# Kernel tuning notes

Hardware: AMD Instinct MI355X
Metric: run time of the kernel (lower is better)

Reference implementation:

```python
import jax, jax.numpy as jnp
import numpy as np

DT = 0.01  # integration timestep of the Euler-discretized plant


def setup_inputs() -> dict:
    key = jax.random.key(0)
    ks = jax.random.split(key, 8)
    B, T, n, m, c = 2048, 128, 16, 8, 4
    state0 = jax.random.normal(ks[0], (B, n), dtype=jnp.float32)
    controls = jax.random.normal(ks[1], (B, T, c), dtype=jnp.float32)
    obs = jax.random.normal(ks[2], (B, T, m), dtype=jnp.float32)
    A = jax.random.normal(ks[3], (n, n), dtype=jnp.float32) * 0.3
    Bc = jax.random.normal(ks[4], (n, c), dtype=jnp.float32)
    H = jax.random.normal(ks[5], (m, n), dtype=jnp.float32) * 0.5
    Mq = jax.random.normal(ks[6], (n, n), dtype=jnp.float32)
    Q = (Mq @ Mq.T) * (0.01 / n) + 0.01 * jnp.eye(n, dtype=jnp.float32)  # SPD process noise
    Mr = jax.random.normal(ks[7], (m, m), dtype=jnp.float32)
    R = (Mr @ Mr.T) * (0.1 / m) + 0.1 * jnp.eye(m, dtype=jnp.float32)    # SPD obs noise
    P0 = jnp.broadcast_to(jnp.eye(n, dtype=jnp.float32), (B, n, n))       # initial covariance
    return {"state0": state0, "P0": P0, "controls": controls, "obs": obs,
            "A": A, "Bc": Bc, "H": H, "Q": Q, "R": R}


def reference(state0, P0, controls, obs, A, Bc, H, Q, R):
    # Batched Kalman filter (predict + update) over T steps, then RTS smoothing.
    B, n = state0.shape
    T = controls.shape[1]
    I = jnp.eye(n, dtype=state0.dtype)
    F = I + DT * A  # constant Jacobian of the linear Euler plant

    def plant(s, u):  # s: [B,n], u: [B,c]
        return s + DT * (s @ A.T + u @ Bc.T)

    def filt_step(carry, xs):
        s_f, P_f = carry          # filtered state/cov from previous step
        u, y = xs                 # [B,c], [B,m]
        # --- prediction: state_ = plant(s), P_ = F P F^T + Q ---
        s_p = plant(s_f, u)
        P_p = jnp.einsum('ij,bjk,lk->bil', F, P_f, F) + Q
        # --- filtering: K = P H^T (H P H^T + R)^{-1} ---
        PHt = jnp.einsum('bij,kj->bik', P_p, H)       # [B,n,m]
        S = jnp.einsum('ki,bim->bkm', H, PHt) + R      # [B,m,m]
        K = PHt @ jnp.linalg.inv(S)                    # [B,n,m]
        innov = y - s_p @ H.T                          # obs - obs_pred
        s_new = s_p + jnp.einsum('bnm,bm->bn', K, innov)
        P_new = P_p - jnp.einsum('bnm,mj,bjk->bnk', K, H, P_p)
        return (s_new, P_new), (s_p, P_p, s_new, P_new)

    xs = (jnp.swapaxes(controls, 0, 1), jnp.swapaxes(obs, 0, 1))  # [T,B,...]
    _, (s_p_seq, P_p_seq, s_f_seq, P_f_seq) = jax.lax.scan(filt_step, (state0, P0), xs)

    # --- RTS smoothing: A = P_f F^T P_p^{-1}; backward recursion ---
    def smooth_step(carry, xs):
        s_s_next, P_s_next = carry
        s_f, P_f, s_p_next, P_p_next = xs
        Pinv = jnp.linalg.inv(P_p_next)
        G = jnp.einsum('bij,kj,bkl->bil', P_f, F, Pinv)   # smoothing gain [B,n,n]
        s_s = s_f + jnp.einsum('bnm,bm->bn', G, s_s_next - s_p_next)
        P_s = P_f + G @ (P_s_next - P_p_next) @ jnp.swapaxes(G, -1, -2)
        return (s_s, P_s), s_s

    xs_s = (s_f_seq[:-1], P_f_seq[:-1], s_p_seq[1:], P_p_seq[1:])
    init = (s_f_seq[-1], P_f_seq[-1])
    _, s_s_seq = jax.lax.scan(smooth_step, init, xs_s, reverse=True)
    s_s_all = jnp.concatenate([s_s_seq, s_f_seq[-1:]], axis=0)  # [T,B,n]
    return jnp.swapaxes(s_s_all, 0, 1)  # smoothed states [B,T,n]
```

## Files before the change

### kernel.cpp

```cpp
#include <hip/hip_runtime.h>

#define NB 2048
#define TS 128
#define NS 16
#define MS 8
#define CS 4
#define DTC 0.01f

#define K_OFF 0
#define K_SZ (TS*NS*MS)
#define G_OFF (K_OFF + K_SZ)
#define G_SZ ((TS-1)*NS*NS)
#define PP_OFF (G_OFF + G_SZ)
#define PP_SZ (TS*NS*NS)
#define PF_OFF (PP_OFF + PP_SZ)
#define PF_SZ (TS*NS*NS)
#define A_OFF (PF_OFF + PF_SZ)
#define A_SZ (TS*NS*NS)
#define M_OFF (A_OFF + A_SZ)
#define M_SZ (TS*NS*CS)

#define GSHFL(v, k) __shfl((v), ((tid & 48) | (k)), 64)

__global__ __launch_bounds__(256) void cov_kernel(
    const float* __restrict__ Ag, const float* __restrict__ Hg,
    const float* __restrict__ Qg, const float* __restrict__ Rg,
    const float* __restrict__ P0g, const float* __restrict__ Bcg,
    float* __restrict__ Kw, float* __restrict__ Ppw, float* __restrict__ Pfw,
    float* __restrict__ Aw, float* __restrict__ Mw)
{
    __shared__ float Fs[NS][NS], Qs[NS][NS];
    __shared__ float Hs[MS][NS], HFs[MS][NS], QHt[NS][MS];
    __shared__ float Rs[MS][MS], HBcs[MS][CS], Bcs[NS][CS];
    __shared__ float Pf[NS][NS], Pp[NS][NS], TP[NS][NS];
    __shared__ float PHt[NS][MS], HP[MS][NS], Ks[NS][MS];
    __shared__ float Sg[MS][MS];

    const int tid = threadIdx.x;
    const int i = tid >> 4, j = tid & 15;

    float Fri[NS];
#pragma unroll
    for (int k = 0; k < NS; ++k) Fri[k] = ((i == k) ? 1.f : 0.f) + DTC * Ag[i*NS + k];

    Fs[i][j] = ((i == j) ? 1.f : 0.f) + DTC * Ag[tid];
    Qs[i][j] = Qg[tid];
    if (tid < MS*NS) Hs[tid >> 4][tid & 15] = Hg[tid];
    if (tid < MS*MS) Rs[tid >> 3][tid & 7] = Rg[tid];
    if (tid < NS*CS) Bcs[tid >> 2][tid & 3] = Bcg[tid];
    Pf[i][j] = P0g[tid];
    __syncthreads();

    if (tid < MS*NS) {
        const int a = tid >> 4, k = tid & 15;
        float acc = 0.f;
#pragma unroll
        for (int m = 0; m < NS; ++m) acc += Hs[a][m] * Fs[m][k];
        HFs[a][k] = acc;
    } else {
        const int e = tid - 128, ii = e >> 3, b = e & 7;
        float acc = 0.f;
#pragma unroll
        for (int k = 0; k < NS; ++k) acc += Qs[ii][k] * Hs[b][k];
        QHt[ii][b] = acc;
    }
    if (tid < MS*CS) {
        const int r = tid >> 2, c = tid & 3;
        float acc = 0.f;
#pragma unroll
        for (int k = 0; k < NS; ++k) acc += Hs[r][k] * Bcs[k][c];
        HBcs[r][c] = acc;
    }
    __syncthreads();

    for (int t = 0; t < TS; ++t) {
        {
            float a0 = 0.f, a1 = 0.f;
#pragma unroll
            for (int k = 0; k < NS; k += 2) { a0 += Fri[k]*Pf[k][j]; a1 += Fri[k+1]*Pf[k+1][j]; }
            TP[i][j] = a0 + a1;
        }
        __syncthreads();

        if (tid < NS*MS) {
            const int ii = tid >> 3, l = tid & 7;
            float b0 = QHt[ii][l], b1 = 0.f;
#pragma unroll
            for (int k = 0; k < NS; k += 2) { b0 += TP[ii][k]*HFs[l][k]; b1 += TP[ii][k+1]*HFs[l][k+1]; }
            PHt[ii][l] = b0 + b1;
        } else {
            const int e = tid - 128;
#pragma unroll
            for (int rep = 0; rep < 2; ++rep) {
                const int en = e + rep*128;
                const int ie = en >> 4, je = en & 15;
                float c0 = Qs[ie][je], c1 = 0.f;
#pragma unroll
                for (int k = 0; k < NS; k += 2) { c0 += TP[ie][k]*Fs[je][k]; c1 += TP[ie][k+1]*Fs[je][k+1]; }
                const float ppv = c0 + c1;
                Pp[ie][je] = ppv;
                Ppw[t*(NS*NS) + en] = ppv;
            }
        }
        __syncthreads();

        if (tid < 64) {
            const int r = tid >> 3, c = tid & 7;
            float v = Rs[r][c];
#pragma unroll
            for (int k = 0; k < NS; ++k) v += Hs[r][k] * PHt[k][c];
            Sg[r][c] = v;
        } else if (tid >= 128) {
            const int e = tid - 128, m = e >> 4, jj = e & 15;
            float v = 0.f;
#pragma unroll
            for (int k = 0; k < NS; ++k) v += Hs[m][k] * Pp[k][jj];
            HP[m][jj] = v;
        }
        __syncthreads();

        if (tid < 128) {
            const int ii = tid >> 3, m = tid & 7;
            float Sr[MS][MS];
#pragma unroll
            for (int a = 0; a < MS; ++a) {
                const float4 x0 = *(const float4*)&Sg[a][0];
                const float4 x1 = *(const float4*)&Sg[a][4];
                Sr[a][0]=x0.x; Sr[a][1]=x0.y; Sr[a][2]=x0.z; Sr[a][3]=x0.w;
                Sr[a][4]=x1.x; Sr[a][5]=x1.y; Sr[a][6]=x1.z; Sr[a][7]=x1.w;
            }
            float rds[MS];
#pragma unroll
            for (int p = 0; p < MS; ++p) {
                const float rd = 1.f / Sr[p][p]; rds[p] = rd;
#pragma unroll
                for (int r = p+1; r < MS; ++r) {
                    const float f = Sr[r][p] * rd; Sr[r][p] = f;
#pragma unroll
                    for (int c = p+1; c < MS; ++c) Sr[r][c] -= f * Sr[p][c];
                }
            }
            float yv[MS];
#pragma unroll
            for (int r = 0; r < MS; ++r) {
                float v = (r == m) ? 1.f : 0.f;
#pragma unroll
                for (int c = 0; c < r; ++c) v -= Sr[r][c] * yv[c];
                yv[r] = v;
            }
            float xv[MS];
#pragma unroll
            for (int r = MS-1; r >= 0; --r) {
                float v = yv[r];
#pragma unroll
                for (int c = r+1; c < MS; ++c) v -= Sr[r][c] * xv[c];
                xv[r] = v * rds[r];
            }
            const float4 p0 = *(const float4*)&PHt[ii][0];
            const float4 p1 = *(const float4*)&PHt[ii][4];
            float kv = p0.x*xv[0] + p0.y*xv[1] + p0.z*xv[2] + p0.w*xv[3]
                     + p1.x*xv[4] + p1.y*xv[5] + p1.z*xv[6] + p1.w*xv[7];
            Ks[ii][m] = kv;
            Kw[t*(NS*MS) + tid] = kv;
        }
        __syncthreads();

        {
            float kr[MS];
            *(float4*)&kr[0] = *(const float4*)&Ks[i][0];
            *(float4*)&kr[4] = *(const float4*)&Ks[i][4];
            float pf = Pp[i][j], av = Fs[i][j];
#pragma unroll
            for (int m = 0; m < MS; ++m) { pf -= kr[m] * HP[m][j]; av -= kr[m] * HFs[m][j]; }
            Pf[i][j] = pf;
            Pfw[t*(NS*NS) + tid] = pf;
            Aw[t*(NS*NS) + tid] = av;
            if (tid < NS*CS) {
                const int ri = tid >> 2, c = tid & 3;
                float mv = Bcs[ri][c];
#pragma unroll
                for (int m = 0; m < MS; ++m) mv -= Ks[ri][m] * HBcs[m][c];
                Mw[t*(NS*CS) + tid] = DTC * mv;
            }
        }
        __syncthreads();
    }
}

__global__ __launch_bounds__(256) void g_kernel(
    const float* __restrict__ Ag,
    const float* __restrict__ Ppw, const float* __restrict__ Pfw,
    float* __restrict__ Gw)
{
    const int t   = blockIdx.x;
    const int tid = threadIdx.x;
    const int r = tid >> 4, cl = tid & 15;

    __shared__ float aug0[NS][NS], aug1[NS][NS], Pfs[NS][NS], Ws[NS][NS];

    float Frc[NS];
#pragma unroll
    for (int k = 0; k < NS; ++k) Frc[k] = ((cl == k) ? 1.f : 0.f) + DTC * Ag[cl*NS + k];

    aug0[r][cl] = Ppw[(t+1)*(NS*NS) + tid];
    aug1[r][cl] = (r == cl) ? 1.f : 0.f;
    Pfs[r][cl]  = Pfw[t*(NS*NS) + tid];
    __syncthreads();

    for (int p = 0; p < NS; ++p) {
        const float a0 = aug0[r][cl], a1 = aug1[r][cl];
        const float d  = aug0[p][p];
        const float pa = aug0[p][cl], pb = aug1[p][cl];
        const float f  = aug0[r][p];
        __syncthreads();
        const float rd = 1.f / d;
        if (r == p) { aug0[r][cl] = pa * rd;       aug1[r][cl] = pb * rd; }
        else        { const float frd = f * rd;
                      aug0[r][cl] = a0 - frd * pa; aug1[r][cl] = a1 - frd * pb; }
        __syncthreads();
    }

    float w0 = 0.f, w1 = 0.f;
#pragma unroll
    for (int k = 0; k < NS; k += 2) { w0 += Pfs[r][k]*Frc[k]; w1 += Pfs[r][k+1]*Frc[k+1]; }
    Ws[r][cl] = w0 + w1;
    __syncthreads();

    float g0 = 0.f, g1 = 0.f;
#pragma unroll
    for (int k = 0; k < NS; k += 2) { g0 += Ws[r][k]*aug1[k][cl]; g1 += Ws[r][k+1]*aug1[k+1][cl]; }
    Gw[t*(NS*NS) + tid] = g0 + g1;
}

__global__ __launch_bounds__(256) void prep_kernel(
    const float* __restrict__ ctrl, const float* __restrict__ obsg,
    const float* __restrict__ Kw, const float* __restrict__ Mw,
    float* __restrict__ outp)
{
    const int g = blockIdx.x * 256 + threadIdx.x;
    const int b = g >> 11;
    const int rem = g & 2047;
    const int t = rem >> 4, i = rem & 15;

    const float4 u  = *(const float4*)(ctrl + (size_t)b*TS*CS + t*CS);
    const float4 y0 = *(const float4*)(obsg + (size_t)b*TS*MS + t*MS);
    const float4 y1 = *(const float4*)(obsg + (size_t)b*TS*MS + t*MS + 4);
    const float4 mr = *(const float4*)(Mw + t*(NS*CS) + i*CS);
    const float4 k0 = *(const float4*)(Kw + t*(NS*MS) + i*MS);
    const float4 k1 = *(const float4*)(Kw + t*(NS*MS) + i*MS + 4);

    float v = mr.x*u.x + mr.y*u.y + mr.z*u.z + mr.w*u.w;
    v += k0.x*y0.x + k0.y*y0.y + k0.z*y0.z + k0.w*y0.w;
    v += k1.x*y1.x + k1.y*y1.y + k1.z*y1.z + k1.w*y1.w;
    outp[g] = v;
}

__global__ __launch_bounds__(256) void fwd_kernel(
    const float* __restrict__ s0g, const float* __restrict__ Aw,
    float* __restrict__ outp)
{
    const int tid  = threadIdx.x;
    const int lane = tid & 15;
    const int b    = blockIdx.x * 16 + (tid >> 4);

    float s = s0g[b*NS + lane];
    float* ob = outp + (size_t)b * TS * NS;

    float4 a0 = *(const float4*)(Aw + lane*NS);
    float4 a1 = *(const float4*)(Aw + lane*NS + 4);
    float4 a2 = *(const float4*)(Aw + lane*NS + 8);
    float4 a3 = *(const float4*)(Aw + lane*NS + 12);

    for (int t = 0; t < TS; ++t) {
        const float bt = ob[t*NS + lane];
        float4 n0, n1, n2, n3;
        if (t + 1 < TS) {
            const float* ap = Aw + (t+1)*(NS*NS) + lane*NS;
            n0 = *(const float4*)(ap);     n1 = *(const float4*)(ap + 4);
            n2 = *(const float4*)(ap + 8); n3 = *(const float4*)(ap + 12);
        }
        float p0 = bt, p1 = 0.f, p2 = 0.f, p3 = 0.f;
        p0 += a0.x*GSHFL(s,0)  + a0.y*GSHFL(s,1);
        p1 += a0.z*GSHFL(s,2)  + a0.w*GSHFL(s,3);
        p2 += a1.x*GSHFL(s,4)  + a1.y*GSHFL(s,5);
        p3 += a1.z*GSHFL(s,6)  + a1.w*GSHFL(s,7);
        p0 += a2.x*GSHFL(s,8)  + a2.y*GSHFL(s,9);
        p1 += a2.z*GSHFL(s,10) + a2.w*GSHFL(s,11);
        p2 += a3.x*GSHFL(s,12) + a3.y*GSHFL(s,13);
        p3 += a3.z*GSHFL(s,14) + a3.w*GSHFL(s,15);
        const float sn = (p0 + p1) + (p2 + p3);
        ob[t*NS + lane] = sn;
        s = sn;
        if (t + 1 < TS) { a0 = n0; a1 = n1; a2 = n2; a3 = n3; }
    }
}

__global__ __launch_bounds__(256) void bwd_kernel(
    const float* __restrict__ Gw, const float* __restrict__ ctrl,
    const float* __restrict__ Ag, const float* __restrict__ Bcg,
    float* __restrict__ outp)
{
    const int tid  = threadIdx.x;
    const int lane = tid & 15;
    const int b    = blockIdx.x * 16 + (tid >> 4);

    float Fi[NS], Bci[CS];
#pragma unroll
    for (int k = 0; k < NS; ++k) Fi[k] = ((lane == k) ? 1.f : 0.f) + DTC * Ag[lane*NS + k];
#pragma unroll
    for (int k = 0; k < CS; ++k) Bci[k] = DTC * Bcg[lane*CS + k];

    const float* up = ctrl + (size_t)b * TS * CS;
    float* ob = outp + (size_t)b * TS * NS;

    float ss = ob[(TS-1)*NS + lane];

    for (int t = TS-2; t >= 0; --t) {
        const float sf = ob[t*NS + lane];

        const float4 u = *(const float4*)(up + (t+1)*CS);
        float p0 = Bci[0]*u.x + Bci[1]*u.y, p1 = Bci[2]*u.z + Bci[3]*u.w, p2 = 0.f, p3 = 0.f;
#pragma unroll
        for (int k = 0; k < NS; k += 4) {
            p0 += Fi[k  ] * GSHFL(sf, k);
            p1 += Fi[k+1] * GSHFL(sf, k+1);
            p2 += Fi[k+2] * GSHFL(sf, k+2);
            p3 += Fi[k+3] * GSHFL(sf, k+3);
        }
        const float diff = ss - ((p0 + p1) + (p2 + p3));

        const float4 g0 = *(const float4*)(Gw + t*(NS*NS) + lane*NS);
        const float4 g1 = *(const float4*)(Gw + t*(NS*NS) + lane*NS + 4);
        const float4 g2 = *(const float4*)(Gw + t*(NS*NS) + lane*NS + 8);
        const float4 g3 = *(const float4*)(Gw + t*(NS*NS) + lane*NS + 12);

        float a0 = g0.x*GSHFL(diff,0)  + g0.y*GSHFL(diff,1);
        a0      += g0.z*GSHFL(diff,2)  + g0.w*GSHFL(diff,3);
        float a1 = g1.x*GSHFL(diff,4)  + g1.y*GSHFL(diff,5);
        a1      += g1.z*GSHFL(diff,6)  + g1.w*GSHFL(diff,7);
        float a2 = g2.x*GSHFL(diff,8)  + g2.y*GSHFL(diff,9);
        a2      += g2.z*GSHFL(diff,10) + g2.w*GSHFL(diff,11);
        float a3 = g3.x*GSHFL(diff,12) + g3.y*GSHFL(diff,13);
        a3      += g3.z*GSHFL(diff,14) + g3.w*GSHFL(diff,15);

        const float sn = sf + ((a0 + a1) + (a2 + a3));
        ob[t*NS + lane] = sn;
        ss = sn;
    }
}

extern "C" void kernel_launch(void* const* d_in, const int* in_sizes, int n_in,
                              void* d_out, int out_size, void* d_ws, size_t ws_size,
                              hipStream_t stream)
{
    (void)out_size; (void)ws_size;

    const float *s0 = nullptr, *P0 = nullptr, *ctrl = nullptr, *obs = nullptr;
    const float *A = nullptr, *Bc = nullptr, *H = nullptr, *Q = nullptr, *R = nullptr;
    for (int idx = 0; idx < n_in; ++idx) {
        const float* p = (const float*)d_in[idx];
        switch (in_sizes[idx]) {
            case NB*NS:        s0   = p; break;
            case NB*NS*NS:     P0   = p; break;
            case NB*TS*CS:     ctrl = p; break;
            case NB*TS*MS:     obs  = p; break;
            case MS*NS:        H    = p; break;
            case NS*NS:        if (!A)  A  = p; else Q = p; break;
            case MS*MS:        if (!Bc) Bc = p; else R = p; break;
            default: break;
        }
    }

    float* ws  = (float*)d_ws;
    float* Kw  = ws + K_OFF;
    float* Gw  = ws + G_OFF;
    float* Ppw = ws + PP_OFF;
    float* Pfw = ws + PF_OFF;
    float* Aw  = ws + A_OFF;
    float* Mw  = ws + M_OFF;
    float* out = (float*)d_out;

    hipLaunchKernelGGL(cov_kernel,  dim3(1),            dim3(256), 0, stream,
                       A, H, Q, R, P0, Bc, Kw, Ppw, Pfw, Aw, Mw);
    hipLaunchKernelGGL(g_kernel,    dim3(TS-1),         dim3(256), 0, stream, A, Ppw, Pfw, Gw);
    hipLaunchKernelGGL(prep_kernel, dim3(NB*TS*NS/256), dim3(256), 0, stream, ctrl, obs, Kw, Mw, out);
    hipLaunchKernelGGL(fwd_kernel,  dim3(NB/16),        dim3(256), 0, stream, s0, Aw, out);
    hipLaunchKernelGGL(bwd_kernel,  dim3(NB/16),        dim3(256), 0, stream, Gw, ctrl, A, Bc, out);
}
```

Baseline: 360.9 us.

## Shorten covariance step dependency chain and prefetch per-step loads in scans

The covariance kernel now computes the innovation covariance S directly from the filtered covariance, as HF·Pf·(HF)^T + (H Q H^T + R). The constant term is precomputed once as Rbar. This removes one barrier-separated phase per timestep, and the HP product moves into the idle threads of the solve phase. The forward and backward state kernels also prefetch the next timestep's value from global memory one iteration ahead, hiding load latency on the serial recurrence. The reassociated S is algebraically equivalent but may differ slightly in rounding.

```diff
diff --git a/kernel.cpp b/kernel.cpp
--- a/kernel.cpp
+++ b/kernel.cpp
@@ -31,8 +31,8 @@
 {
     __shared__ float Fs[NS][NS], Qs[NS][NS];
     __shared__ float Hs[MS][NS], HFs[MS][NS], QHt[NS][MS];
-    __shared__ float Rs[MS][MS], HBcs[MS][CS], Bcs[NS][CS];
-    __shared__ float Pf[NS][NS], Pp[NS][NS], TP[NS][NS];
+    __shared__ float Rs[MS][MS], Rbar[MS][MS], HBcs[MS][CS], Bcs[NS][CS];
+    __shared__ float Pf[NS][NS], Pp[NS][NS], TP[NS][NS], Ws[MS][NS];
     __shared__ float PHt[NS][MS], HP[MS][NS], Ks[NS][MS];
     __shared__ float Sg[MS][MS];
 
@@ -73,49 +73,51 @@
     }
     __syncthreads();
 
+    if (tid < MS*MS) {
+        const int r = tid >> 3, c = tid & 7;
+        float acc = Rs[r][c];
+#pragma unroll
+        for (int k = 0; k < NS; ++k) acc += Hs[r][k] * QHt[k][c];
+        Rbar[r][c] = acc;
+    }
+    __syncthreads();
+
     for (int t = 0; t < TS; ++t) {
         {
             float a0 = 0.f, a1 = 0.f;
 #pragma unroll
             for (int k = 0; k < NS; k += 2) { a0 += Fri[k]*Pf[k][j]; a1 += Fri[k+1]*Pf[k+1][j]; }
             TP[i][j] = a0 + a1;
-        }
-        __syncthreads();
-
-        if (tid < NS*MS) {
-            const int ii = tid >> 3, l = tid & 7;
-            float b0 = QHt[ii][l], b1 = 0.f;
-#pragma unroll
-            for (int k = 0; k < NS; k += 2) { b0 += TP[ii][k]*HFs[l][k]; b1 += TP[ii][k+1]*HFs[l][k+1]; }
-            PHt[ii][l] = b0 + b1;
-        } else {
-            const int e = tid - 128;
-#pragma unroll
-            for (int rep = 0; rep < 2; ++rep) {
-                const int en = e + rep*128;
-                const int ie = en >> 4, je = en & 15;
-                float c0 = Qs[ie][je], c1 = 0.f;
-#pragma unroll
-                for (int k = 0; k < NS; k += 2) { c0 += TP[ie][k]*Fs[je][k]; c1 += TP[ie][k+1]*Fs[je][k+1]; }
-                const float ppv = c0 + c1;
-                Pp[ie][je] = ppv;
-                Ppw[t*(NS*NS) + en] = ppv;
-            }
-        }
-        __syncthreads();
-
-        if (tid < 64) {
-            const int r = tid >> 3, c = tid & 7;
-            float v = Rs[r][c];
-#pragma unroll
-            for (int k = 0; k < NS; ++k) v += Hs[r][k] * PHt[k][c];
-            Sg[r][c] = v;
-        } else if (tid >= 128) {
-            const int e = tid - 128, m = e >> 4, jj = e & 15;
-            float v = 0.f;
-#pragma unroll
-            for (int k = 0; k < NS; ++k) v += Hs[m][k] * Pp[k][jj];
-            HP[m][jj] = v;
+            if (tid < MS*NS) {
+                const int a = tid >> 4, jj = tid & 15;
+                float w0 = 0.f, w1 = 0.f;
+#pragma unroll
+                for (int k = 0; k < NS; k += 2) { w0 += HFs[a][k]*Pf[k][jj]; w1 += HFs[a][k+1]*Pf[k+1][jj]; }
+                Ws[a][jj] = w0 + w1;
+            }
+        }
+        __syncthreads();
+
+        {
+            float c0 = Qs[i][j], c1 = 0.f;
+#pragma unroll
+            for (int k = 0; k < NS; k += 2) { c0 += TP[i][k]*Fs[j][k]; c1 += TP[i][k+1]*Fs[j][k+1]; }
+            const float ppv = c0 + c1;
+            Pp[i][j] = ppv;
+            Ppw[t*(NS*NS) + tid] = ppv;
+            if (tid < NS*MS) {
+                const int ii = tid >> 3, l = tid & 7;
+                float b0 = QHt[ii][l], b1 = 0.f;
+#pragma unroll
+                for (int k = 0; k < NS; k += 2) { b0 += TP[ii][k]*HFs[l][k]; b1 += TP[ii][k+1]*HFs[l][k+1]; }
+                PHt[ii][l] = b0 + b1;
+            } else if (tid < 192) {
+                const int e = tid - 128, r = e >> 3, c = e & 7;
+                float s0 = Rbar[r][c], s1 = 0.f;
+#pragma unroll
+                for (int k = 0; k < NS; k += 2) { s0 += Ws[r][k]*HFs[c][k]; s1 += Ws[r][k+1]*HFs[c][k+1]; }
+                Sg[r][c] = s0 + s1;
+            }
         }
         __syncthreads();
 
@@ -162,6 +164,12 @@
                      + p1.x*xv[4] + p1.y*xv[5] + p1.z*xv[6] + p1.w*xv[7];
             Ks[ii][m] = kv;
             Kw[t*(NS*MS) + tid] = kv;
+        } else {
+            const int e = tid - 128, m = e >> 4, jj = e & 15;
+            float v = 0.f;
+#pragma unroll
+            for (int k = 0; k < NS; ++k) v += Hs[m][k] * Pp[k][jj];
+            HP[m][jj] = v;
         }
         __syncthreads();
 
@@ -270,14 +278,16 @@
     float4 a1 = *(const float4*)(Aw + lane*NS + 4);
     float4 a2 = *(const float4*)(Aw + lane*NS + 8);
     float4 a3 = *(const float4*)(Aw + lane*NS + 12);
+    float bt = ob[lane];
 
     for (int t = 0; t < TS; ++t) {
-        const float bt = ob[t*NS + lane];
         float4 n0, n1, n2, n3;
+        float btn;
         if (t + 1 < TS) {
             const float* ap = Aw + (t+1)*(NS*NS) + lane*NS;
             n0 = *(const float4*)(ap);     n1 = *(const float4*)(ap + 4);
             n2 = *(const float4*)(ap + 8); n3 = *(const float4*)(ap + 12);
+            btn = ob[(t+1)*NS + lane];
         }
         float p0 = bt, p1 = 0.f, p2 = 0.f, p3 = 0.f;
         p0 += a0.x*GSHFL(s,0)  + a0.y*GSHFL(s,1);
@@ -291,7 +301,7 @@
         const float sn = (p0 + p1) + (p2 + p3);
         ob[t*NS + lane] = sn;
         s = sn;
-        if (t + 1 < TS) { a0 = n0; a1 = n1; a2 = n2; a3 = n3; }
+        if (t + 1 < TS) { a0 = n0; a1 = n1; a2 = n2; a3 = n3; bt = btn; }
     }
 }
 
@@ -314,9 +324,11 @@
     float* ob = outp + (size_t)b * TS * NS;
 
     float ss = ob[(TS-1)*NS + lane];
+    float sf = ob[(TS-2)*NS + lane];
 
     for (int t = TS-2; t >= 0; --t) {
-        const float sf = ob[t*NS + lane];
+        float sfn;
+        if (t > 0) sfn = ob[(t-1)*NS + lane];
 
         const float4 u = *(const float4*)(up + (t+1)*CS);
         float p0 = Bci[0]*u.x + Bci[1]*u.y, p1 = Bci[2]*u.z + Bci[3]*u.w, p2 = 0.f, p3 = 0.f;
@@ -346,6 +358,7 @@
         const float sn = sf + ((a0 + a1) + (a2 + a3));
         ob[t*NS + lane] = sn;
         ss = sn;
+        sf = sfn;
     }
 }
 
```

Result: no change. 368.0 us (+1.9%).
